# Kernel tuning notes

Measured on AMD Instinct MI355X. Metric: run time of the kernel, lower is better.

## Reference

```python
import jax, jax.numpy as jnp
import numpy as np
from jax import lax

EPS = 1e-5


def _conv3x3(inp, w):
    # NCHW input, OIHW kernel, VALID padding, stride 1 (matches nn.Conv2d(k=3, s=1, p=0))
    return lax.conv_general_dilated(inp, w, (1, 1), 'VALID',
                                    dimension_numbers=('NCHW', 'OIHW', 'NCHW'))


def _bn(h, gamma, beta, mean, var):
    # inference-mode BatchNorm2d
    inv = gamma / jnp.sqrt(var + EPS)
    return h * inv[None, :, None, None] + (beta - mean * inv)[None, :, None, None]


def _xcorr_depthwise(zf, xf):
    # per-sample, per-channel sliding cross-correlation: template zf over search xf
    B, C, Hz, Wz = zf.shape
    _, _, Hx, Wx = xf.shape
    xr = xf.reshape(1, B * C, Hx, Wx)
    kr = zf.reshape(B * C, 1, Hz, Wz)
    out = lax.conv_general_dilated(xr, kr, (1, 1), 'VALID',
                                   feature_group_count=B * C,
                                   dimension_numbers=('NCHW', 'OIHW', 'NCHW'))
    return out.reshape(B, C, out.shape[2], out.shape[3])


def setup_inputs() -> dict:
    key = jax.random.key(0)
    ks = jax.random.split(key, 12)
    B, Cin, Ch = 64, 256, 256
    z = jax.random.normal(ks[0], (B, Cin, 16, 16), dtype=jnp.float32)
    x = jax.random.normal(ks[1], (B, Cin, 32, 32), dtype=jnp.float32)
    # conv weights ~ N(0, 0.01) as in _initialize_weights
    w_z = 0.01 * jax.random.normal(ks[2], (Ch, Cin, 3, 3), dtype=jnp.float32)
    w_x = 0.01 * jax.random.normal(ks[3], (Ch, Cin, 3, 3), dtype=jnp.float32)
    gamma_z = 0.5 + jax.random.uniform(ks[4], (Ch,), dtype=jnp.float32)
    beta_z = 0.1 * jax.random.normal(ks[5], (Ch,), dtype=jnp.float32)
    mean_z = 0.1 * jax.random.normal(ks[6], (Ch,), dtype=jnp.float32)
    var_z = 0.5 + jax.random.uniform(ks[7], (Ch,), dtype=jnp.float32)
    gamma_x = 0.5 + jax.random.uniform(ks[8], (Ch,), dtype=jnp.float32)
    beta_x = 0.1 * jax.random.normal(ks[9], (Ch,), dtype=jnp.float32)
    mean_x = 0.1 * jax.random.normal(ks[10], (Ch,), dtype=jnp.float32)
    var_x = 0.5 + jax.random.uniform(ks[11], (Ch,), dtype=jnp.float32)
    return {'z': z, 'x': x, 'w_z': w_z, 'w_x': w_x,
            'gamma_z': gamma_z, 'beta_z': beta_z, 'mean_z': mean_z, 'var_z': var_z,
            'gamma_x': gamma_x, 'beta_x': beta_x, 'mean_x': mean_x, 'var_x': var_x}


def reference(z, x, w_z, w_x, gamma_z, beta_z, mean_z, var_z,
              gamma_x, beta_x, mean_x, var_x):
    zf = _bn(_conv3x3(z, w_z), gamma_z, beta_z, mean_z, var_z)   # [B,C,14,14]
    xf = _bn(_conv3x3(x, w_x), gamma_x, beta_x, mean_x, var_x)   # [B,C,30,30]
    return _xcorr_depthwise(zf, xf)                               # [B,C,17,17]
```

## Files before the change

kernel.cpp:

```cpp
#include <hip/hip_runtime.h>
#include <cstdint>
#include <cstddef>

typedef _Float16 f16;
typedef _Float16 half4 __attribute__((ext_vector_type(4)));
typedef _Float16 half8 __attribute__((ext_vector_type(8)));
typedef float f32x4 __attribute__((ext_vector_type(4)));

#define BN_EPS 1e-5f

static constexpr size_t OFF_XB  = 0;
static constexpr size_t OFF_ZB  = 33554432;
static constexpr size_t OFF_WX  = 41943040;
static constexpr size_t OFF_WZ  = 43122688;
static constexpr size_t OFF_BNX = 44302336;
static constexpr size_t OFF_BNZ = 44304384;
static constexpr size_t OFF_XFH = 44306432;
static constexpr size_t OFF_ZFH = 75763712;

__global__ __launch_bounds__(256) void prep_all(
    const float* __restrict__ x, const float* __restrict__ z,
    const float* __restrict__ w_x, const float* __restrict__ w_z,
    const float* __restrict__ gx, const float* __restrict__ bx,
    const float* __restrict__ mx, const float* __restrict__ vx,
    const float* __restrict__ gz, const float* __restrict__ bz,
    const float* __restrict__ mz, const float* __restrict__ vz,
    f16* __restrict__ xb, f16* __restrict__ zb,
    f16* __restrict__ wxA, f16* __restrict__ wzA,
    float* __restrict__ bnx, float* __restrict__ bnz) {
  __shared__ float tile[64][33];
  const int bid = blockIdx.x;
  const int tid = threadIdx.x;
  if (bid < 12288) {
    const float* src; f16* dst; int lw, r;
    if (bid < 8192) { src = x; dst = xb; lw = 5; r = bid; }
    else            { src = z; dst = zb; lw = 4; r = bid - 8192; }
    const int W = 1 << lw;
    const int c0 = (r & 3) << 6;
    const int h = (r >> 2) & (W - 1);
    const int b = (r >> 2) >> lw;
    const float* sp = src + (size_t)(((b << 8) + c0) << lw << lw) + ((size_t)h << lw);
    const int n = W << 6;
    for (int i = tid; i < n; i += 256) {
      int cl = i >> lw, w = i & (W - 1);
      tile[cl][w] = sp[(size_t)cl << lw << lw | w];
    }
    __syncthreads();
    f16* dp = dst + ((size_t)((b << lw) + h) << lw << 8) + c0;
    for (int i = tid; i < n; i += 256) {
      int w = i >> 6, cl = i & 63;
      dp[(w << 8) + cl] = (f16)tile[cl][w];
    }
  } else if (bid < 16896) {
    int r = bid - 12288;
    const float* src = (r < 2304) ? w_x : w_z;
    f16* dst = (r < 2304) ? wxA : wzA;
    int rr = (r < 2304) ? r : r - 2304;
    int idx = rr * 256 + tid;
    int cin = idx & 255, cout = (idx >> 8) & 255, khw = idx >> 16;
    dst[idx] = (f16)src[(cout * 256 + cin) * 9 + khw];
  } else {
    int c = tid;
    float iv = gx[c] / sqrtf(vx[c] + BN_EPS);
    bnx[c] = iv;
    bnx[256 + c] = bx[c] - mx[c] * iv;
    float iz = gz[c] / sqrtf(vz[c] + BN_EPS);
    bnz[c] = iz;
    bnz[256 + c] = bz[c] - mz[c] * iz;
  }
}

__device__ __forceinline__ void gl_lds16(const f16* g, f16* l) {
  __builtin_amdgcn_global_load_lds((__attribute__((address_space(1))) void*)g,
                                   (__attribute__((address_space(3))) void*)l, 16, 0, 0);
}

__global__ __launch_bounds__(256, 4) void conv_gemm_u(
    const f16* __restrict__ xb, const f16* __restrict__ zb,
    const f16* __restrict__ wx, const f16* __restrict__ wz,
    const float* __restrict__ bnx, const float* __restrict__ bnz,
    f16* __restrict__ xfh, f16* __restrict__ zfh) {
  __shared__ f16 As[128 * 64];
  __shared__ f16 Bs[128 * 64];
  const int bid = blockIdx.x;
  const f16* inp; const f16* wA; const float* bn; f16* out;
  int nblk, mblk, HIN, WIN, WOUT, NPIX, WPAD, OPLANE;
  if (bid < 900) {
    inp = xb; wA = wx; bn = bnx; out = xfh;
    nblk = bid >> 1; mblk = bid & 1;
    HIN = 32; WIN = 32; WOUT = 30; NPIX = 900; WPAD = 32; OPLANE = 960;
  } else {
    int r = bid - 900;
    inp = zb; wA = wz; bn = bnz; out = zfh;
    nblk = r >> 1; mblk = r & 1;
    HIN = 16; WIN = 16; WOUT = 14; NPIX = 196; WPAD = 16; OPLANE = 224;
  }
  const int tid = threadIdx.x;
  const int wid = tid >> 6, lane = tid & 63;
  const int wm = (wid >> 1) << 6, wn = (wid & 1) << 6;
  const int q = lane >> 4, lm = lane & 15;
  const int sr = lane >> 3, sc = lane & 7;
  const int swz = (sc ^ sr) << 3;
  const int mbase = mblk << 7;

  int arow[4], brow[4];
#pragma unroll
  for (int l = 0; l < 4; ++l) {
    int rr = (wid << 5) + (l << 3) + sr;
    arow[l] = ((mbase + rr) << 8) + swz;
    int n = (nblk << 7) + rr;
    int b = n / NPIX, rem = n - b * NPIX;
    int oh = rem / WOUT, ow = rem - oh * WOUT;
    brow[l] = (((b * HIN + oh) * WIN + ow) << 8) + swz;
  }

  f32x4 acc[4][4] = {};
  const int cA0 = (q ^ (lm & 7)) << 3;

  for (int kt = 0; kt < 36; ++kt) {
    const int khw = kt >> 2;
    const int cin0 = (kt & 3) << 6;
    const int kh = khw / 3, kw = khw - kh * 3;
    const int wofs = (khw << 16) + cin0;
    const int iofs = ((kh * WIN + kw) << 8) + cin0;
#pragma unroll
    for (int l = 0; l < 4; ++l) {
      const int ldso = ((wid << 5) + (l << 3)) << 6;
      gl_lds16(wA + wofs + arow[l], As + ldso);
      gl_lds16(inp + iofs + brow[l], Bs + ldso);
    }
    __syncthreads();
#pragma unroll
    for (int h = 0; h < 2; ++h) {
      const int co = cA0 ^ (h << 5);
      half8 af[4], bf[4];
#pragma unroll
      for (int f = 0; f < 4; ++f) {
        af[f] = *(const half8*)&As[((wm + (f << 4) + lm) << 6) + co];
        bf[f] = *(const half8*)&Bs[((wn + (f << 4) + lm) << 6) + co];
      }
#pragma unroll
      for (int fm = 0; fm < 4; ++fm)
#pragma unroll
        for (int fn = 0; fn < 4; ++fn)
          acc[fm][fn] =
              __builtin_amdgcn_mfma_f32_16x16x32_f16(af[fm], bf[fn], acc[fm][fn], 0, 0, 0);
    }
    __syncthreads();
  }

#pragma unroll
  for (int fn = 0; fn < 4; ++fn) {
    int n_g = (nblk << 7) + wn + (fn << 4) + lm;
    int b = n_g / NPIX, rem = n_g - b * NPIX;
    int oh = rem / WOUT, ow = rem - oh * WOUT;
    f16* op = out + (size_t)(b << 8) * OPLANE + oh * WPAD + ow;
#pragma unroll
    for (int fm = 0; fm < 4; ++fm) {
      int m0 = mbase + wm + (fm << 4) + (q << 2);
#pragma unroll
      for (int rg = 0; rg < 4; ++rg) {
        int m = m0 + rg;
        op[(size_t)m * OPLANE] = (f16)(acc[fm][fn][rg] * bn[m] + bn[256 + m]);
      }
    }
  }
}

static constexpr int XST = 40;
static constexpr int XCH = 30 * XST;
static constexpr int ZCH = 14 * 16;

__global__ __launch_bounds__(256) void xcorr_dw3(const f16* __restrict__ zfh,
                                                 const f16* __restrict__ xfh,
                                                 float* __restrict__ out) {
  __shared__ f16 xs[3 * XCH];
  __shared__ f16 zs[3 * ZCH];
  const int t = threadIdx.x;
  const int ch0 = blockIdx.x * 3;

  for (int i = t; i < 360; i += 256) {
    int ch = i / 120, rem = i - ch * 120;
    int row = rem >> 2, col = (rem & 3) << 3;
    if (ch0 + ch < 16384)
      *(half8*)(xs + ch * XCH + row * XST + col) =
          *(const half8*)(xfh + (size_t)(ch0 + ch) * 960 + row * 32 + col);
  }
  for (int i = t; i < 84; i += 256) {
    int ch = i / 28, rem = i - ch * 28;
    if (ch0 + ch < 16384)
      *(half8*)(zs + ch * ZCH + rem * 8) =
          *(const half8*)(zfh + (size_t)(ch0 + ch) * 224 + rem * 8);
  }
  __syncthreads();

  int lc = t / 85;
  int r = t - lc * 85;
  const bool ok = (lc < 3) && (ch0 + lc < 16384);
  if (lc > 2) lc = 2;
  const int oy = r / 5, oxq = r - oy * 5, ox0 = oxq * 4;
  const f16* xbp = xs + lc * XCH;
  const f16* zbp = zs + lc * ZCH;

  float acc[4] = {0.f, 0.f, 0.f, 0.f};

#pragma unroll 2
  for (int u = 0; u < 14; ++u) {
    float xr[20];
#pragma unroll
    for (int k = 0; k < 5; ++k) {
      half4 h = *(const half4*)(xbp + (oy + u) * XST + ox0 + k * 4);
#pragma unroll
      for (int e = 0; e < 4; ++e) xr[k * 4 + e] = (float)h[e];
    }
    float zc[14];
    {
      half8 z0 = *(const half8*)(zbp + u * 16);
      half8 z1 = *(const half8*)(zbp + u * 16 + 8);
#pragma unroll
      for (int e = 0; e < 8; ++e) zc[e] = (float)z0[e];
#pragma unroll
      for (int e = 0; e < 6; ++e) zc[8 + e] = (float)z1[e];
    }
#pragma unroll
    for (int v = 0; v < 14; ++v)
#pragma unroll
      for (int j = 0; j < 4; ++j) acc[j] = fmaf(zc[v], xr[v + j], acc[j]);
  }

  if (ok) {
    float* op = out + (size_t)(ch0 + lc) * 289 + oy * 17;
#pragma unroll
    for (int j = 0; j < 4; ++j) {
      int ox = ox0 + j;
      if (ox < 17) op[ox] = acc[j];
    }
  }
}

extern "C" void kernel_launch(void* const* d_in, const int* in_sizes, int n_in,
                              void* d_out, int out_size, void* d_ws, size_t ws_size,
                              hipStream_t stream) {
  const float* z = (const float*)d_in[0];
  const float* x = (const float*)d_in[1];
  const float* w_z = (const float*)d_in[2];
  const float* w_x = (const float*)d_in[3];
  const float* gamma_z = (const float*)d_in[4];
  const float* beta_z = (const float*)d_in[5];
  const float* mean_z = (const float*)d_in[6];
  const float* var_z = (const float*)d_in[7];
  const float* gamma_x = (const float*)d_in[8];
  const float* beta_x = (const float*)d_in[9];
  const float* mean_x = (const float*)d_in[10];
  const float* var_x = (const float*)d_in[11];

  char* ws = (char*)d_ws;
  f16* xb = (f16*)(ws + OFF_XB);
  f16* zb = (f16*)(ws + OFF_ZB);
  f16* wxA = (f16*)(ws + OFF_WX);
  f16* wzA = (f16*)(ws + OFF_WZ);
  float* bnx = (float*)(ws + OFF_BNX);
  float* bnz = (float*)(ws + OFF_BNZ);
  f16* xfh = (f16*)(ws + OFF_XFH);
  f16* zfh = (f16*)(ws + OFF_ZFH);
  float* out = (float*)d_out;

  prep_all<<<16897, 256, 0, stream>>>(x, z, w_x, w_z,
                                      gamma_x, beta_x, mean_x, var_x,
                                      gamma_z, beta_z, mean_z, var_z,
                                      xb, zb, wxA, wzA, bnx, bnz);

  conv_gemm_u<<<1096, 256, 0, stream>>>(xb, zb, wxA, wzA, bnx, bnz, xfh, zfh);

  xcorr_dw3<<<(16384 + 2) / 3, 256, 0, stream>>>(zfh, xfh, out);
}
```

Before: 331.2 us.

## Retile conv GEMM to 256x64 blocks with 32x32x16 MFMA and 2 waves

The implicit-GEMM convolution kernel now gives each block all 256 output channels against 64 pixels, instead of splitting M into two 128-row blocks. Each of the two waves computes a 128x64 tile using 32x32x16 MFMA instructions. The kernel-tile loop order also changes to iterate cin blocks outermost. This removes the duplicated input tile loads across M blocks and lowers LDS fragment reads per MFMA. In exchange there are only 2 waves per block and a larger weight tile load per step, and the extra accumulator registers may limit latency hiding.

```diff
diff --git a/kernel.cpp b/kernel.cpp
--- a/kernel.cpp
+++ b/kernel.cpp
@@ -5,7 +5,7 @@
 typedef _Float16 f16;
 typedef _Float16 half4 __attribute__((ext_vector_type(4)));
 typedef _Float16 half8 __attribute__((ext_vector_type(8)));
-typedef float f32x4 __attribute__((ext_vector_type(4)));
+typedef float f32x16 __attribute__((ext_vector_type(16)));
 
 #define BN_EPS 1e-5f
 
@@ -75,93 +75,89 @@
                                    (__attribute__((address_space(3))) void*)l, 16, 0, 0);
 }
 
-__global__ __launch_bounds__(256, 4) void conv_gemm_u(
+__global__ __launch_bounds__(128, 2) void conv_gemm_v2(
     const f16* __restrict__ xb, const f16* __restrict__ zb,
     const f16* __restrict__ wx, const f16* __restrict__ wz,
     const float* __restrict__ bnx, const float* __restrict__ bnz,
     f16* __restrict__ xfh, f16* __restrict__ zfh) {
-  __shared__ f16 As[128 * 64];
-  __shared__ f16 Bs[128 * 64];
+  __shared__ f16 As[256 * 64];
+  __shared__ f16 Bs[64 * 64];
   const int bid = blockIdx.x;
   const f16* inp; const f16* wA; const float* bn; f16* out;
-  int nblk, mblk, HIN, WIN, WOUT, NPIX, WPAD, OPLANE;
+  int nblk, HIN, WIN, WOUT, NPIX, WPAD, OPLANE;
   if (bid < 900) {
-    inp = xb; wA = wx; bn = bnx; out = xfh;
-    nblk = bid >> 1; mblk = bid & 1;
+    inp = xb; wA = wx; bn = bnx; out = xfh; nblk = bid;
     HIN = 32; WIN = 32; WOUT = 30; NPIX = 900; WPAD = 32; OPLANE = 960;
   } else {
-    int r = bid - 900;
-    inp = zb; wA = wz; bn = bnz; out = zfh;
-    nblk = r >> 1; mblk = r & 1;
+    inp = zb; wA = wz; bn = bnz; out = zfh; nblk = bid - 900;
     HIN = 16; WIN = 16; WOUT = 14; NPIX = 196; WPAD = 16; OPLANE = 224;
   }
-  const int tid = threadIdx.x;
-  const int wid = tid >> 6, lane = tid & 63;
-  const int wm = (wid >> 1) << 6, wn = (wid & 1) << 6;
-  const int q = lane >> 4, lm = lane & 15;
-  const int sr = lane >> 3, sc = lane & 7;
-  const int swz = (sc ^ sr) << 3;
-  const int mbase = mblk << 7;
-
-  int arow[4], brow[4];
+  const int t = threadIdx.x;
+  const int w = t >> 6;
+  const int L = t & 63;
+  const int rbase = (w << 3) + (L >> 3);
+  const int swz = (((L & 7) ^ (rbase & 7)) << 3);
+  const int abase = (rbase << 8) + swz;
+
+  int ib[4];
 #pragma unroll
   for (int l = 0; l < 4; ++l) {
-    int rr = (wid << 5) + (l << 3) + sr;
-    arow[l] = ((mbase + rr) << 8) + swz;
-    int n = (nblk << 7) + rr;
+    int p = (l << 4) + rbase;
+    int n = (nblk << 6) + p;
     int b = n / NPIX, rem = n - b * NPIX;
     int oh = rem / WOUT, ow = rem - oh * WOUT;
-    brow[l] = (((b * HIN + oh) * WIN + ow) << 8) + swz;
-  }
-
-  f32x4 acc[4][4] = {};
-  const int cA0 = (q ^ (lm & 7)) << 3;
+    ib[l] = (((b * HIN + oh) * WIN + ow) << 8) + swz;
+  }
+
+  f32x16 acc[4][2] = {};
 
   for (int kt = 0; kt < 36; ++kt) {
-    const int khw = kt >> 2;
-    const int cin0 = (kt & 3) << 6;
+    const int cinb = kt / 9;
+    const int khw = kt - cinb * 9;
     const int kh = khw / 3, kw = khw - kh * 3;
-    const int wofs = (khw << 16) + cin0;
-    const int iofs = ((kh * WIN + kw) << 8) + cin0;
-#pragma unroll
-    for (int l = 0; l < 4; ++l) {
-      const int ldso = ((wid << 5) + (l << 3)) << 6;
-      gl_lds16(wA + wofs + arow[l], As + ldso);
-      gl_lds16(inp + iofs + brow[l], Bs + ldso);
-    }
+    const int wofs = (khw << 16) + (cinb << 6);
+    const int iofs = ((kh * WIN + kw) << 8) + (cinb << 6);
+#pragma unroll
+    for (int l = 0; l < 16; ++l)
+      gl_lds16(wA + wofs + (l << 12) + abase, As + ((((l << 4) + (w << 3))) << 6));
+#pragma unroll
+    for (int l = 0; l < 4; ++l)
+      gl_lds16(inp + iofs + ib[l], Bs + ((((l << 4) + (w << 3))) << 6));
     __syncthreads();
-#pragma unroll
-    for (int h = 0; h < 2; ++h) {
-      const int co = cA0 ^ (h << 5);
-      half8 af[4], bf[4];
-#pragma unroll
-      for (int f = 0; f < 4; ++f) {
-        af[f] = *(const half8*)&As[((wm + (f << 4) + lm) << 6) + co];
-        bf[f] = *(const half8*)&Bs[((wn + (f << 4) + lm) << 6) + co];
-      }
-#pragma unroll
-      for (int fm = 0; fm < 4; ++fm)
-#pragma unroll
-        for (int fn = 0; fn < 4; ++fn)
-          acc[fm][fn] =
-              __builtin_amdgcn_mfma_f32_16x16x32_f16(af[fm], bf[fn], acc[fm][fn], 0, 0, 0);
+
+#pragma unroll
+    for (int ks = 0; ks < 4; ++ks) {
+      const int ch = ((((ks << 1) + (L >> 5)) ^ (L & 7)) << 3);
+      half8 af[4], bf[2];
+#pragma unroll
+      for (int mt = 0; mt < 4; ++mt)
+        af[mt] = *(const half8*)&As[(((w << 7) + (mt << 5) + (L & 31)) << 6) + ch];
+#pragma unroll
+      for (int nt = 0; nt < 2; ++nt)
+        bf[nt] = *(const half8*)&Bs[(((nt << 5) + (L & 31)) << 6) + ch];
+#pragma unroll
+      for (int mt = 0; mt < 4; ++mt)
+#pragma unroll
+        for (int nt = 0; nt < 2; ++nt)
+          acc[mt][nt] =
+              __builtin_amdgcn_mfma_f32_32x32x16_f16(af[mt], bf[nt], acc[mt][nt], 0, 0, 0);
     }
     __syncthreads();
   }
 
 #pragma unroll
-  for (int fn = 0; fn < 4; ++fn) {
-    int n_g = (nblk << 7) + wn + (fn << 4) + lm;
+  for (int nt = 0; nt < 2; ++nt) {
+    int n_g = (nblk << 6) + (nt << 5) + (L & 31);
     int b = n_g / NPIX, rem = n_g - b * NPIX;
     int oh = rem / WOUT, ow = rem - oh * WOUT;
     f16* op = out + (size_t)(b << 8) * OPLANE + oh * WPAD + ow;
 #pragma unroll
-    for (int fm = 0; fm < 4; ++fm) {
-      int m0 = mbase + wm + (fm << 4) + (q << 2);
-#pragma unroll
-      for (int rg = 0; rg < 4; ++rg) {
-        int m = m0 + rg;
-        op[(size_t)m * OPLANE] = (f16)(acc[fm][fn][rg] * bn[m] + bn[256 + m]);
+    for (int mt = 0; mt < 4; ++mt) {
+      const int mb = (w << 7) + (mt << 5) + ((L >> 5) << 2);
+#pragma unroll
+      for (int rg = 0; rg < 16; ++rg) {
+        int m = mb + (rg & 3) + ((rg >> 2) << 3);
+        op[(size_t)m * OPLANE] = (f16)(acc[mt][nt][rg] * bn[m] + bn[256 + m]);
       }
     }
   }
@@ -270,7 +266,7 @@
                                       gamma_z, beta_z, mean_z, var_z,
                                       xb, zb, wxA, wzA, bnx, bnz);
 
-  conv_gemm_u<<<1096, 256, 0, stream>>>(xb, zb, wxA, wzA, bnx, bnz, xfh, zfh);
+  conv_gemm_v2<<<1096, 128, 0, stream>>>(xb, zb, wxA, wzA, bnx, bnz, xfh, zfh);
 
   xcorr_dw3<<<(16384 + 2) / 3, 256, 0, stream>>>(zfh, xfh, out);
 }
```

New measurement: 365.0 us. 1.1x slower.
